# Kernel tuning notes

Hardware: AMD Instinct MI355X
Metric: run time of the kernel (lower is better)

## Reference

```python
import jax, jax.numpy as jnp
import numpy as np

E, T, I, O = 8, 8192, 2048, 4096  # experts, total_tokens, in_features, out_features


def setup_inputs() -> dict:
    key = jax.random.key(0)
    k1, k2, k3 = jax.random.split(key, 3)
    inputs = jax.random.normal(k1, (T, I), dtype=jnp.float32)
    # lecun_normal-style scale for the (E, I, O) kernel (fan_in = I)
    kernel = jax.random.normal(k2, (E, I, O), dtype=jnp.float32) * (1.0 / np.float32(np.sqrt(I)))
    # nonzero bias so the ragged bias-expansion path is exercised
    bias = jax.random.normal(k3, (E, O), dtype=jnp.float32) * 0.02
    # tokens are sorted by expert; equal groups summing exactly to T
    group_sizes = jnp.full((E,), T // E, dtype=jnp.int32)
    return {"inputs": inputs, "group_sizes": group_sizes, "kernel": kernel, "bias": bias}


def reference(inputs, group_sizes, kernel, bias):
    # Ragged grouped GEMM: row block g of `inputs` (size group_sizes[g]) is
    # multiplied by kernel[g] of shape (I, O). Matches _ragged_dot with
    # out_first=False: contraction dims ((1,), (1,)), rhs group dim 0.
    out = jax.lax.ragged_dot(inputs, kernel, group_sizes)  # (T, O)
    # Per-group bias add: bias[e] broadcast over that expert's token block.
    expert_ids = jnp.repeat(jnp.arange(E), group_sizes, total_repeat_length=T)
    return out + bias[expert_ids]
```

## Files before the change

kernel.cpp:

```cpp
#include <hip/hip_runtime.h>


typedef short bf16x8 __attribute__((ext_vector_type(8)));
typedef float f32x4 __attribute__((ext_vector_type(4)));
typedef unsigned short u16x8 __attribute__((ext_vector_type(8)));

constexpr int Ecnt = 8;
constexpr int Ttok = 8192;
constexpr int Ifeat = 2048;
constexpr int Ofeat = 4096;
constexpr int BM = 128, BN = 128, BK = 32;

__device__ __forceinline__ unsigned short f2bf(float f) {
  unsigned u = __float_as_uint(f);
  unsigned r = (u + 0x7FFFu + ((u >> 16) & 1u)) >> 16;
  return (unsigned short)r;
}

__global__ __launch_bounds__(256) void cvt_a(const float* __restrict__ src,
                                             unsigned short* __restrict__ dst) {
  size_t i = ((size_t)blockIdx.x * 256 + threadIdx.x) * 8;
  float4 f0 = *(const float4*)(src + i);
  float4 f1 = *(const float4*)(src + i + 4);
  u16x8 v;
  v[0] = f2bf(f0.x); v[1] = f2bf(f0.y); v[2] = f2bf(f0.z); v[3] = f2bf(f0.w);
  v[4] = f2bf(f1.x); v[5] = f2bf(f1.y); v[6] = f2bf(f1.z); v[7] = f2bf(f1.w);
  *(u16x8*)(dst + i) = v;
}

__global__ __launch_bounds__(256) void cvt_b(const float* __restrict__ src,
                                             unsigned short* __restrict__ dst) {
  constexpr int LDST = 129;
  __shared__ float tile[64 * LDST];
  const int e = blockIdx.z;
  const int i0 = blockIdx.y * 64;
  const int o0 = blockIdx.x * 128;
  const int tid = threadIdx.x;

  {
    const int tx = tid & 31, ty = tid >> 5;
    const float* s = src + ((size_t)e * Ifeat + i0) * Ofeat + o0 + tx * 4;
#pragma unroll
    for (int r = 0; r < 8; ++r) {
      int i = r * 8 + ty;
      float4 f = *(const float4*)(s + (size_t)i * Ofeat);
      float* l = tile + i * LDST + tx * 4;
      l[0] = f.x; l[1] = f.y; l[2] = f.z; l[3] = f.w;
    }
  }
  __syncthreads();
  {
    const int ic = (tid & 7) * 8;
    const int oc = tid >> 3;
#pragma unroll
    for (int p = 0; p < 4; ++p) {
      int o = p * 32 + oc;
      u16x8 v;
#pragma unroll
      for (int j = 0; j < 8; ++j) v[j] = f2bf(tile[(ic + j) * LDST + o]);
      unsigned short* d =
          dst + ((size_t)e * Ofeat + o0 + o) * Ifeat + i0 + ic;
      *(u16x8*)d = v;
    }
  }
}

__device__ __forceinline__ void ld16(const unsigned short* g, unsigned short* l) {
  __builtin_amdgcn_global_load_lds(
      (const __attribute__((address_space(1))) unsigned int*)g,
      (__attribute__((address_space(3))) unsigned int*)l, 16, 0, 0);
}

__global__ __launch_bounds__(256) void moe_gemm(
    const unsigned short* __restrict__ A,
    const unsigned short* __restrict__ Bt,
    const int* __restrict__ gs,
    const float* __restrict__ bias,
    float* __restrict__ C) {
  __shared__ unsigned short lA[BM * BK];
  __shared__ unsigned short lB[BN * BK];

  const int tid = threadIdx.x;
  const int bid = blockIdx.x;
  const int eg = bid >> 8;
  const int rt = (bid & 255) & 7;
  const int ct = (bid & 255) >> 3;
  const int row0 = eg * 1024 + rt * BM;
  const int col0 = ct * BN;

  int e = 0;
  {
    int cum = 0;
#pragma unroll
    for (int g = 0; g < Ecnt; ++g) {
      int s = gs[g];
      if (row0 >= cum + s) { cum += s; e = g + 1; }
    }
  }

  const unsigned short* Ag = A + (size_t)row0 * Ifeat;
  const unsigned short* Bg = Bt + ((size_t)e * Ofeat + col0) * Ifeat;

  const int wave = tid >> 6, lane = tid & 63;
  const int wm = (wave >> 1) * 64, wn = (wave & 1) * 64;
  const int lrow = lane & 15;
  const int kb = (lane >> 4) * 8;

  const int c0 = tid, c1 = tid + 256;
  const unsigned short* a0 = Ag + (size_t)(c0 >> 2) * Ifeat + (c0 & 3) * 8;
  const unsigned short* a1 = Ag + (size_t)(c1 >> 2) * Ifeat + (c1 & 3) * 8;
  const unsigned short* b0 = Bg + (size_t)(c0 >> 2) * Ifeat + (c0 & 3) * 8;
  const unsigned short* b1 = Bg + (size_t)(c1 >> 2) * Ifeat + (c1 & 3) * 8;
  unsigned short* la0 = lA + c0 * 8;
  unsigned short* la1 = lA + c1 * 8;
  unsigned short* lb0 = lB + c0 * 8;
  unsigned short* lb1 = lB + c1 * 8;

  f32x4 acc[4][4];
#pragma unroll
  for (int i = 0; i < 4; ++i)
#pragma unroll
    for (int j = 0; j < 4; ++j) acc[i][j] = (f32x4){0.f, 0.f, 0.f, 0.f};

  for (int k0 = 0; k0 < Ifeat; k0 += BK) {
    ld16(a0 + k0, la0);
    ld16(a1 + k0, la1);
    ld16(b0 + k0, lb0);
    ld16(b1 + k0, lb1);
    __syncthreads();

    bf16x8 af[4], bf[4];
#pragma unroll
    for (int mt = 0; mt < 4; ++mt)
      af[mt] = *(const bf16x8*)(lA + (wm + mt * 16 + lrow) * BK + kb);
#pragma unroll
    for (int nt = 0; nt < 4; ++nt)
      bf[nt] = *(const bf16x8*)(lB + (wn + nt * 16 + lrow) * BK + kb);

#pragma unroll
    for (int mt = 0; mt < 4; ++mt)
#pragma unroll
      for (int nt = 0; nt < 4; ++nt)
        acc[mt][nt] = __builtin_amdgcn_mfma_f32_16x16x32_bf16(
            af[mt], bf[nt], acc[mt][nt], 0, 0, 0);

    __syncthreads();
  }

  const int r0 = (lane >> 4) * 4;
  const int cc = lane & 15;
  const float* be = bias + (size_t)e * Ofeat;
#pragma unroll
  for (int mt = 0; mt < 4; ++mt) {
    const int row = row0 + wm + mt * 16 + r0;
#pragma unroll
    for (int nt = 0; nt < 4; ++nt) {
      const int col = col0 + wn + nt * 16 + cc;
      const float b = be[col];
      float* Cp = C + (size_t)row * Ofeat + col;
#pragma unroll
      for (int r = 0; r < 4; ++r) Cp[(size_t)r * Ofeat] = acc[mt][nt][r] + b;
    }
  }
}

extern "C" void kernel_launch(void* const* d_in, const int* in_sizes, int n_in,
                              void* d_out, int out_size, void* d_ws, size_t ws_size,
                              hipStream_t stream) {
  const float* inputs = (const float*)d_in[0];
  const int* group_sizes = (const int*)d_in[1];
  const float* kern = (const float*)d_in[2];
  const float* bias = (const float*)d_in[3];
  float* out = (float*)d_out;

  unsigned short* Abf = (unsigned short*)d_ws;
  unsigned short* Bbf = Abf + (size_t)Ttok * Ifeat;

  cvt_a<<<(Ttok * (size_t)Ifeat) / (8 * 256), 256, 0, stream>>>(inputs, Abf);
  cvt_b<<<dim3(Ofeat / 128, Ifeat / 64, Ecnt), 256, 0, stream>>>(kern, Bbf);

  moe_gemm<<<Ttok / BM * (Ofeat / BN), 256, 0, stream>>>(Abf, Bbf, group_sizes,
                                                         bias, out);
}
```

Before: 638.2 us.

## Double K tile, XOR-swizzle LDS layout, and remap blocks for XCD locality

Raises BK from 32 to 64, so each barrier pair now covers two MFMA k-steps and the loop runs half as many iterations. It adds an XOR swizzle on the 16-byte chunk index when loading into LDS, so the fragment reads avoid bank conflicts. It also changes the block-to-tile mapping so each XCD (bid&7) owns a contiguous set of column tiles and walks all row tiles, which is meant to improve L2 reuse of B. LDS per block doubles to 32KB, which may lower occupancy.

```diff
diff --git a/kernel.cpp b/kernel.cpp
--- a/kernel.cpp
+++ b/kernel.cpp
@@ -9,7 +9,7 @@
 constexpr int Ttok = 8192;
 constexpr int Ifeat = 2048;
 constexpr int Ofeat = 4096;
-constexpr int BM = 128, BN = 128, BK = 32;
+constexpr int BM = 128, BN = 128, BK = 64;
 
 __device__ __forceinline__ unsigned short f2bf(float f) {
   unsigned u = __float_as_uint(f);
@@ -36,7 +36,6 @@
   const int i0 = blockIdx.y * 64;
   const int o0 = blockIdx.x * 128;
   const int tid = threadIdx.x;
-
   {
     const int tx = tid & 31, ty = tid >> 5;
     const float* s = src + ((size_t)e * Ifeat + i0) * Ofeat + o0 + tx * 4;
@@ -82,10 +81,11 @@
 
   const int tid = threadIdx.x;
   const int bid = blockIdx.x;
-  const int eg = bid >> 8;
-  const int rt = (bid & 255) & 7;
-  const int ct = (bid & 255) >> 3;
-  const int row0 = eg * 1024 + rt * BM;
+  const int xcd = bid & 7;
+  const int j = bid >> 3;
+  const int ct = xcd * 4 + (j >> 6);
+  const int rtile = j & 63;
+  const int row0 = rtile * BM;
   const int col0 = ct * BN;
 
   int e = 0;
@@ -104,45 +104,60 @@
   const int wave = tid >> 6, lane = tid & 63;
   const int wm = (wave >> 1) * 64, wn = (wave & 1) * 64;
   const int lrow = lane & 15;
-  const int kb = (lane >> 4) * 8;
+  const int kg = lane >> 4;
+  const int xr = lrow & 7;
 
-  const int c0 = tid, c1 = tid + 256;
-  const unsigned short* a0 = Ag + (size_t)(c0 >> 2) * Ifeat + (c0 & 3) * 8;
-  const unsigned short* a1 = Ag + (size_t)(c1 >> 2) * Ifeat + (c1 & 3) * 8;
-  const unsigned short* b0 = Bg + (size_t)(c0 >> 2) * Ifeat + (c0 & 3) * 8;
-  const unsigned short* b1 = Bg + (size_t)(c1 >> 2) * Ifeat + (c1 & 3) * 8;
-  unsigned short* la0 = lA + c0 * 8;
-  unsigned short* la1 = lA + c1 * 8;
-  unsigned short* lb0 = lB + c0 * 8;
-  unsigned short* lb1 = lB + c1 * 8;
+  const int64_t koff[4] = {
+      (int64_t)((tid + 0) >> 3) * Ifeat + (((tid + 0) & 7) ^ (((tid + 0) >> 3) & 7)) * 8,
+      (int64_t)((tid + 256) >> 3) * Ifeat + (((tid + 256) & 7) ^ (((tid + 256) >> 3) & 7)) * 8,
+      (int64_t)((tid + 512) >> 3) * Ifeat + (((tid + 512) & 7) ^ (((tid + 512) >> 3) & 7)) * 8,
+      (int64_t)((tid + 768) >> 3) * Ifeat + (((tid + 768) & 7) ^ (((tid + 768) >> 3) & 7)) * 8};
+  const unsigned short* asrc[4] = {Ag + koff[0], Ag + koff[1], Ag + koff[2],
+                                   Ag + koff[3]};
+  const unsigned short* bsrc[4] = {Bg + koff[0], Bg + koff[1], Bg + koff[2],
+                                   Bg + koff[3]};
+  unsigned short* adst[4] = {lA + (size_t)tid * 8, lA + (size_t)(tid + 256) * 8,
+                             lA + (size_t)(tid + 512) * 8,
+                             lA + (size_t)(tid + 768) * 8};
+  unsigned short* bdst[4] = {lB + (size_t)tid * 8, lB + (size_t)(tid + 256) * 8,
+                             lB + (size_t)(tid + 512) * 8,
+                             lB + (size_t)(tid + 768) * 8};
 
   f32x4 acc[4][4];
 #pragma unroll
   for (int i = 0; i < 4; ++i)
 #pragma unroll
-    for (int j = 0; j < 4; ++j) acc[i][j] = (f32x4){0.f, 0.f, 0.f, 0.f};
+    for (int jj = 0; jj < 4; ++jj) acc[i][jj] = (f32x4){0.f, 0.f, 0.f, 0.f};
 
   for (int k0 = 0; k0 < Ifeat; k0 += BK) {
-    ld16(a0 + k0, la0);
-    ld16(a1 + k0, la1);
-    ld16(b0 + k0, lb0);
-    ld16(b1 + k0, lb1);
+#pragma unroll
+    for (int p = 0; p < 4; ++p) ld16(asrc[p] + k0, adst[p]);
+#pragma unroll
+    for (int p = 0; p < 4; ++p) ld16(bsrc[p] + k0, bdst[p]);
     __syncthreads();
 
-    bf16x8 af[4], bf[4];
 #pragma unroll
-    for (int mt = 0; mt < 4; ++mt)
-      af[mt] = *(const bf16x8*)(lA + (wm + mt * 16 + lrow) * BK + kb);
+    for (int s = 0; s < 2; ++s) {
+      bf16x8 af[4], bf[4];
 #pragma unroll
-    for (int nt = 0; nt < 4; ++nt)
-      bf[nt] = *(const bf16x8*)(lB + (wn + nt * 16 + lrow) * BK + kb);
-
+      for (int mt = 0; mt < 4; ++mt) {
+        const int r = wm + mt * 16 + lrow;
+        const int slot = (s * 4 + kg) ^ xr;
+        af[mt] = *(const bf16x8*)(lA + r * BK + slot * 8);
+      }
 #pragma unroll
-    for (int mt = 0; mt < 4; ++mt)
+      for (int nt = 0; nt < 4; ++nt) {
+        const int r = wn + nt * 16 + lrow;
+        const int slot = (s * 4 + kg) ^ xr;
+        bf[nt] = *(const bf16x8*)(lB + r * BK + slot * 8);
+      }
 #pragma unroll
-      for (int nt = 0; nt < 4; ++nt)
-        acc[mt][nt] = __builtin_amdgcn_mfma_f32_16x16x32_bf16(
-            af[mt], bf[nt], acc[mt][nt], 0, 0, 0);
+      for (int mt = 0; mt < 4; ++mt)
+#pragma unroll
+        for (int nt = 0; nt < 4; ++nt)
+          acc[mt][nt] = __builtin_amdgcn_mfma_f32_16x16x32_bf16(
+              af[mt], bf[nt], acc[mt][nt], 0, 0, 0);
+    }
 
     __syncthreads();
   }
```

Result: no change. 630.1 us (-1.3%).
